# Kernel tuning notes

Measured on AMD Instinct MI355X. Metric: run time of the kernel, lower is better.

Reference implementation:

```python
import jax, jax.numpy as jnp
import numpy as np

N_FEAT = 12   # feature_size n -> 2^n-1 = 4095 nonempty subsets
BATCH = 64


def _build_fmat(n):
    # Inclusion-exclusion (Moebius) matrix: column 2k sums f(B) over B >= A_k with
    # even |B \ A_k| (positive part), column 2k+1 over odd |B \ A_k| (negative part).
    masks = np.arange(1, 2 ** n, dtype=np.int64)
    mj, mk = masks[:, None], masks[None, :]
    sub = (mj & mk) == mk            # A_k subset-of A_j
    diff = mj & ~mk
    pc = np.zeros_like(diff)
    for b in range(n):
        pc += (diff >> b) & 1        # popcount(|A_j \ A_k|)
    M = np.zeros((2 ** n - 1, 2 * (2 ** n - 1)), dtype=np.float32)
    M[:, 0::2] = (sub & (pc % 2 == 0)).astype(np.float32)
    M[:, 1::2] = (sub & (pc % 2 == 1)).astype(np.float32)
    return M


def setup_inputs() -> dict:
    key = jax.random.key(0)
    k1, k2, k3 = jax.random.split(key, 3)
    n, B = N_FEAT, BATCH
    xl = jax.random.uniform(k1, (B, n), dtype=jnp.float32)
    xu = xl + (1.0 - xl) * jax.random.uniform(k2, (B, n), dtype=jnp.float32)
    x = jnp.concatenate([xl, xu], axis=1)                          # [B, 2n] lower||upper
    ie_vars = jax.random.uniform(k3, (2 ** n - 2, 1), dtype=jnp.float32) * (0.1 / n)
    singles = jnp.array([2 ** b - 1 for b in range(n)])            # singleton masks -> 1/n
    ie_vars = ie_vars.at[singles, 0].set(1.0 / n)
    fmat = jnp.asarray(_build_fmat(n))                             # [4095, 8190]
    return {"x": x, "ie_vars": ie_vars, "fmat": fmat}


def _subset_products(x, n):
    # feats[:, m-1] = prod_{b in mask m} x[:, b]  (algebraic t-norm over subsets)
    masks = jnp.arange(1, 2 ** n)
    feats = jnp.ones((x.shape[0], 2 ** n - 1), x.dtype)
    for b in range(n):  # n static passes over [B, 2^n-1]
        has_b = ((masks >> b) & 1).astype(bool)
        feats = feats * jnp.where(has_b[None, :], x[:, b:b + 1], jnp.ones((), x.dtype))
    return feats


def _build_FM(ie_vars, n):
    # Monotone fuzzy-measure lattice DP: FM[m] = |v[m]| + max_{b in m} FM[m - 2^b],
    # singletons get just |v|; append mu(full set)=1; clamp to 1.
    v = jnp.abs(ie_vars[:, 0])                    # [2^n - 2]
    nV = 2 ** n - 2
    masks = np.arange(1, 2 ** n - 1)              # static predecessor tables
    preds = np.zeros((nV, n), np.int32)
    valid = np.zeros((nV, n), bool)
    for b in range(n):
        has = ((masks >> b) & 1).astype(bool)
        p = masks - (1 << b) - 1                  # var index of mask with bit b removed
        ok = has & (p >= 0)                       # empty-set predecessor excluded
        preds[:, b] = np.where(ok, p, 0)
        valid[:, b] = ok
    preds_j = jnp.asarray(preds)
    valid_j = jnp.asarray(valid)

    def step(fm, i):
        cand = jnp.where(valid_j[i], fm[preds_j[i]], -jnp.inf)
        mx = jnp.max(cand)
        mx = jnp.where(jnp.isfinite(mx), mx, jnp.zeros((), fm.dtype))
        return fm.at[i].set(v[i] + mx), None

    fm, _ = jax.lax.scan(step, jnp.zeros((nV,), v.dtype), jnp.arange(nV))
    FM = jnp.concatenate([fm, jnp.ones((1,), v.dtype)])
    return jnp.minimum(FM, 1.0)[:, None]          # [2^n - 1, 1]


def reference(x, ie_vars, fmat):
    n = x.shape[1] // 2
    datal, datau = x[:, :n], x[:, n:]
    fl = _subset_products(datal, n)               # [B, 2^n-1]
    fu = _subset_products(datau, n)
    FM = _build_FM(ie_vars, n)                    # [2^n-1, 1]
    fl_mt = fl @ fmat                             # [B, 2*(2^n-1)]
    fu_mt = fu @ fmat
    a = fl_mt[:, 0::2] @ FM                       # [B, 1]
    c = fl_mt[:, 1::2] @ FM
    b_ = fu_mt[:, 0::2] @ FM
    d = fu_mt[:, 1::2] @ FM
    left = jnp.minimum(a - c, b_ - d)
    right = b_ - d
    return left, right
```

## Files before the change

kernel.cpp:

```cpp
#include <hip/hip_runtime.h>


#define NB 12
#define NMASK 4096

__global__ __launch_bounds__(1024) void k_build_w(
    const float* __restrict__ ie_vars, float* __restrict__ W) {
  __shared__ float g[NMASK];
  const int tid = threadIdx.x;

  for (int level = 1; level <= NB; ++level) {
    for (int m = tid; m < NMASK; m += 1024) {
      if (m >= 1 && m <= NMASK - 2 && __popc(m) == level) {
        float best = 0.0f;
#pragma unroll
        for (int b = 0; b < NB; ++b) {
          const int p = m - (1 << b);
          if ((m & (1 << b)) && p >= 1) best = fmaxf(best, g[p]);
        }
        g[m] = fabsf(ie_vars[m - 1]) + best;
      }
    }
    __syncthreads();
  }

  for (int m = tid; m < NMASK; m += 1024) {
    float val;
    if (m == 0)                val = 0.0f;
    else if (m == NMASK - 1)   val = 1.0f;
    else                       val = fminf(g[m], 1.0f);
    g[m] = val;
  }
  __syncthreads();

  for (int b = 0; b < NB; ++b) {
    for (int m = tid; m < NMASK; m += 1024) {
      if (m & (1 << b)) g[m] -= g[m ^ (1 << b)];
    }
    __syncthreads();
  }

  for (int m = tid; m < NMASK; m += 1024) W[m] = g[m];
}

__global__ __launch_bounds__(256) void k_batch(
    const float* __restrict__ x, const float* __restrict__ W,
    float* __restrict__ out) {
  const int b = blockIdx.x;
  const int tid = threadIdx.x;

  __shared__ float xs[24];
  if (tid < 24) xs[tid] = x[b * 24 + tid];
  __syncthreads();

  float lowl[16], lowu[16];
  lowl[0] = 1.0f;
  lowu[0] = 1.0f;
#pragma unroll
  for (int m = 1; m < 16; ++m) {
    const int lb = __ffs(m) - 1;
    lowl[m] = lowl[m & (m - 1)] * xs[lb];
    lowu[m] = lowu[m & (m - 1)] * xs[12 + lb];
  }

  const int hm = tid;
  float hl = 1.0f, hu = 1.0f;
#pragma unroll
  for (int bit = 0; bit < 8; ++bit) {
    if (hm & (1 << bit)) {
      hl *= xs[4 + bit];
      hu *= xs[16 + bit];
    }
  }

  const int base = tid << 4;
  float A = 0.0f, B = 0.0f;
#pragma unroll
  for (int k = 0; k < 16; ++k) {
    const float w = W[base + k];
    A = fmaf(hl * lowl[k], w, A);
    B = fmaf(hu * lowu[k], w, B);
  }

#pragma unroll
  for (int off = 32; off > 0; off >>= 1) {
    A += __shfl_down(A, off);
    B += __shfl_down(B, off);
  }
  __shared__ float rA[4], rB[4];
  const int wave = tid >> 6;
  if ((tid & 63) == 0) {
    rA[wave] = A;
    rB[wave] = B;
  }
  __syncthreads();
  if (tid == 0) {
    const float a = rA[0] + rA[1] + rA[2] + rA[3];
    const float bb = rB[0] + rB[1] + rB[2] + rB[3];
    out[b] = fminf(a, bb);
    out[64 + b] = bb;
  }
}

extern "C" void kernel_launch(void* const* d_in, const int* in_sizes, int n_in,
                              void* d_out, int out_size, void* d_ws,
                              size_t ws_size, hipStream_t stream) {
  const float* x  = (const float*)d_in[0];
  const float* ie = (const float*)d_in[1];
  float* W   = (float*)d_ws;
  float* out = (float*)d_out;

  k_build_w<<<1, 1024, 0, stream>>>(ie, W);
  k_batch<<<64, 256, 0, stream>>>(x, W, out);
}
```

Before: 210.3 us.

## Fuse measure DP and batch reduction into one kernel with level-sorted subset indexing

Merges the two kernels into a single 64-block launch in which every block recomputes the fuzzy-measure DP and Moebius transform in shared memory, then does its own batch row. The DP now walks a combinatorial-number-system index so each popcount level processes only its own masks in one pass, instead of scanning all 4096 masks per level. The first 8 Moebius bit passes stay within each wave, so they need no block barriers. This removes a launch and the workspace round trip, at the cost of repeating the DP redundantly in every block.

```diff
diff --git a/kernel.cpp b/kernel.cpp
--- a/kernel.cpp
+++ b/kernel.cpp
@@ -4,101 +4,140 @@
 #define NB 12
 #define NMASK 4096
 
-__global__ __launch_bounds__(1024) void k_build_w(
-    const float* __restrict__ ie_vars, float* __restrict__ W) {
+__constant__ int d_BIN[156] = {
+    1, 0,  0,  0,   0,   0,   0,   0,   0,  0,  0, 0, 0,
+    1, 1,  0,  0,   0,   0,   0,   0,   0,  0,  0, 0, 0,
+    1, 2,  1,  0,   0,   0,   0,   0,   0,  0,  0, 0, 0,
+    1, 3,  3,  1,   0,   0,   0,   0,   0,  0,  0, 0, 0,
+    1, 4,  6,  4,   1,   0,   0,   0,   0,  0,  0, 0, 0,
+    1, 5, 10, 10,   5,   1,   0,   0,   0,  0,  0, 0, 0,
+    1, 6, 15, 20,  15,   6,   1,   0,   0,  0,  0, 0, 0,
+    1, 7, 21, 35,  35,  21,   7,   1,   0,  0,  0, 0, 0,
+    1, 8, 28, 56,  70,  56,  28,   8,   1,  0,  0, 0, 0,
+    1, 9, 36, 84, 126, 126,  84,  36,   9,  1,  0, 0, 0,
+    1, 10, 45, 120, 210, 252, 210, 120, 45, 10, 1, 0, 0,
+    1, 11, 55, 165, 330, 462, 462, 330, 165, 55, 11, 1, 0
+};
+
+__constant__ int d_OFF[13] = {0, 0, 12, 78, 298, 793, 1585,
+                              2509, 3301, 3796, 4016, 4082, 4094};
+
+__global__ __launch_bounds__(1024) void k_fused(
+    const float* __restrict__ x, const float* __restrict__ ie,
+    float* __restrict__ out) {
   __shared__ float g[NMASK];
+  __shared__ float v[NMASK];
+  __shared__ unsigned short idx[NMASK];
+  __shared__ float xs[24];
+  __shared__ int sBIN[156];
+  __shared__ int sOFF[13];
+  __shared__ float rA[16], rB[16];
+
   const int tid = threadIdx.x;
+  const int lane = tid & 63;
+  const int wave = tid >> 6;
+  const int cbase = wave << 8;
 
-  for (int level = 1; level <= NB; ++level) {
-    for (int m = tid; m < NMASK; m += 1024) {
-      if (m >= 1 && m <= NMASK - 2 && __popc(m) == level) {
-        float best = 0.0f;
+  if (tid < 156) sBIN[tid] = d_BIN[tid];
+  if (tid < 13) sOFF[tid] = d_OFF[tid];
+  if (tid < 24) xs[tid] = x[blockIdx.x * 24 + tid];
+  for (int i = tid; i < NMASK - 2; i += 1024) v[i + 1] = fabsf(ie[i]);
+  __syncthreads();
+
+  for (int m = tid; m < NMASK; m += 1024) {
+    if (m == 0) {
+      g[0] = 0.0f;
+      continue;
+    }
+    int pc = 0, r = 0;
 #pragma unroll
-        for (int b = 0; b < NB; ++b) {
-          const int p = m - (1 << b);
-          if ((m & (1 << b)) && p >= 1) best = fmaxf(best, g[p]);
-        }
-        g[m] = fabsf(ie_vars[m - 1]) + best;
+    for (int b = 0; b < NB; ++b)
+      if (m & (1 << b)) { ++pc; r += sBIN[b * 13 + pc]; }
+    idx[sOFF[pc] + r] = (unsigned short)m;
+  }
+  __syncthreads();
+
+  constexpr int OFF_A[13] = {0, 0, 12, 78, 298, 793, 1585,
+                             2509, 3301, 3796, 4016, 4082, 4094};
+#pragma unroll
+  for (int lv = 1; lv <= 11; ++lv) {
+    const int u = OFF_A[lv] + tid;
+    if (u < OFF_A[lv + 1]) {
+      const int m = (int)idx[u];
+      float best = 0.0f;
+#pragma unroll
+      for (int b = 0; b < NB; ++b) {
+        const int a = (m & (1 << b)) ? (m ^ (1 << b)) : 0;
+        best = fmaxf(best, g[a]);
       }
+      g[m] = v[m] + best;
     }
     __syncthreads();
   }
 
-  for (int m = tid; m < NMASK; m += 1024) {
+#pragma unroll
+  for (int r = 0; r < 4; ++r) {
+    const int m = cbase | (r << 6) | lane;
     float val;
-    if (m == 0)                val = 0.0f;
-    else if (m == NMASK - 1)   val = 1.0f;
-    else                       val = fminf(g[m], 1.0f);
+    if (m == 0)              val = 0.0f;
+    else if (m == NMASK - 1) val = 1.0f;
+    else                     val = fminf(g[m], 1.0f);
     g[m] = val;
   }
+
+#pragma unroll
+  for (int b = 0; b < 8; ++b) {
+#pragma unroll
+    for (int r = 0; r < 2; ++r) {
+      const int j = (r << 6) | lane;
+      const int m =
+          cbase | (((j >> b) << (b + 1)) | (1 << b) | (j & ((1 << b) - 1)));
+      g[m] -= g[m ^ (1 << b)];
+    }
+  }
   __syncthreads();
-
-  for (int b = 0; b < NB; ++b) {
-    for (int m = tid; m < NMASK; m += 1024) {
-      if (m & (1 << b)) g[m] -= g[m ^ (1 << b)];
+#pragma unroll
+  for (int b = 8; b < NB; ++b) {
+    for (int j = tid; j < 2048; j += 1024) {
+      const int m = ((j >> b) << (b + 1)) | (1 << b) | (j & ((1 << b) - 1));
+      g[m] -= g[m ^ (1 << b)];
     }
     __syncthreads();
   }
 
-  for (int m = tid; m < NMASK; m += 1024) W[m] = g[m];
-}
-
-__global__ __launch_bounds__(256) void k_batch(
-    const float* __restrict__ x, const float* __restrict__ W,
-    float* __restrict__ out) {
-  const int b = blockIdx.x;
-  const int tid = threadIdx.x;
-
-  __shared__ float xs[24];
-  if (tid < 24) xs[tid] = x[b * 24 + tid];
-  __syncthreads();
-
-  float lowl[16], lowu[16];
-  lowl[0] = 1.0f;
-  lowu[0] = 1.0f;
-#pragma unroll
-  for (int m = 1; m < 16; ++m) {
-    const int lb = __ffs(m) - 1;
-    lowl[m] = lowl[m & (m - 1)] * xs[lb];
-    lowu[m] = lowu[m & (m - 1)] * xs[12 + lb];
-  }
-
-  const int hm = tid;
+  const float x0l = xs[0], x1l = xs[1], x0u = xs[12], x1u = xs[13];
   float hl = 1.0f, hu = 1.0f;
 #pragma unroll
-  for (int bit = 0; bit < 8; ++bit) {
-    if (hm & (1 << bit)) {
-      hl *= xs[4 + bit];
-      hu *= xs[16 + bit];
+  for (int bit = 0; bit < 10; ++bit) {
+    if (tid & (1 << bit)) {
+      hl *= xs[2 + bit];
+      hu *= xs[14 + bit];
     }
   }
-
-  const int base = tid << 4;
-  float A = 0.0f, B = 0.0f;
-#pragma unroll
-  for (int k = 0; k < 16; ++k) {
-    const float w = W[base + k];
-    A = fmaf(hl * lowl[k], w, A);
-    B = fmaf(hu * lowu[k], w, B);
-  }
+  const float4 w = *reinterpret_cast<const float4*>(&g[tid << 2]);
+  const float l3 = x0l * x1l, u3 = x0u * x1u;
+  float A = hl * (w.x + w.y * x0l + w.z * x1l + w.w * l3);
+  float B = hu * (w.x + w.y * x0u + w.z * x1u + w.w * u3);
 
 #pragma unroll
   for (int off = 32; off > 0; off >>= 1) {
     A += __shfl_down(A, off);
     B += __shfl_down(B, off);
   }
-  __shared__ float rA[4], rB[4];
-  const int wave = tid >> 6;
-  if ((tid & 63) == 0) {
+  if (lane == 0) {
     rA[wave] = A;
     rB[wave] = B;
   }
   __syncthreads();
   if (tid == 0) {
-    const float a = rA[0] + rA[1] + rA[2] + rA[3];
-    const float bb = rB[0] + rB[1] + rB[2] + rB[3];
-    out[b] = fminf(a, bb);
-    out[64 + b] = bb;
+    float a = 0.0f, bb = 0.0f;
+#pragma unroll
+    for (int i = 0; i < 16; ++i) {
+      a += rA[i];
+      bb += rB[i];
+    }
+    out[blockIdx.x] = fminf(a, bb);
+    out[64 + blockIdx.x] = bb;
   }
 }
 
@@ -107,9 +146,7 @@
                               size_t ws_size, hipStream_t stream) {
   const float* x  = (const float*)d_in[0];
   const float* ie = (const float*)d_in[1];
-  float* W   = (float*)d_ws;
   float* out = (float*)d_out;
 
-  k_build_w<<<1, 1024, 0, stream>>>(ie, W);
-  k_batch<<<64, 256, 0, stream>>>(x, W, out);
+  k_fused<<<64, 1024, 0, stream>>>(x, ie, out);
 }
```

New measurement: 171.7 us. 1.22x faster.
